# Kernel tuning notes

Measured on AMD Instinct MI355X. Metric: run time of the kernel, lower is better.

Reference implementation:

```python
import jax, jax.numpy as jnp
import numpy as np

N = 50000      # nodes
E = 800000     # edges (no self-loops; loops added in forward)
D = 128        # input_dim == nb_hidden_gnn
K = 128        # nb_hidden_kernel
EMB = 128      # emb_dim
L = 3          # nb_layer
EPS = 1e-5


def setup_inputs() -> dict:
    key = jax.random.key(0)
    ks = jax.random.split(key, 14)
    x = jax.random.normal(ks[0], (N, D), dtype=jnp.float32)
    src = jax.random.randint(ks[1], (E,), 0, N)
    dst = jax.random.randint(ks[2], (E,), 0, N)
    dst = jnp.where(src == dst, (dst + 1) % N, dst)  # guarantee no self-loops
    edge_index = jnp.stack([src, dst]).astype(jnp.int32)
    edge_attr = jax.random.uniform(ks[3], (E,), dtype=jnp.float32)
    s = 0.05
    # stacked per-layer params (layer 0..L-1): in=out=D for all layers
    lin_w = jax.random.normal(ks[4], (L, D, 2 * D), dtype=jnp.float32) * s
    lin_b = jax.random.normal(ks[5], (L, D), dtype=jnp.float32) * s
    linA_w = jax.random.normal(ks[6], (L, K, 2 * D + 1), dtype=jnp.float32) * s
    linA_b = jax.random.normal(ks[7], (L, K), dtype=jnp.float32) * s
    linB_w = jax.random.normal(ks[8], (L, K), dtype=jnp.float32) * s
    linB_b = jax.random.normal(ks[9], (L,), dtype=jnp.float32) * s
    # batchnorm affine params for layers 1..L-1
    bn_gamma = jnp.ones((L - 1, D), dtype=jnp.float32)
    bn_beta = jnp.zeros((L - 1, D), dtype=jnp.float32)
    final_w = jax.random.normal(ks[10], (EMB, D), dtype=jnp.float32) * s
    final_b = jax.random.normal(ks[11], (EMB,), dtype=jnp.float32) * s
    return {"x": x, "edge_index": edge_index, "edge_attr": edge_attr,
            "lin_w": lin_w, "lin_b": lin_b,
            "linA_w": linA_w, "linA_b": linA_b,
            "linB_w": linB_w, "linB_b": linB_b,
            "bn_gamma": bn_gamma, "bn_beta": bn_beta,
            "final_w": final_w, "final_b": final_b}


def _batchnorm(h, gamma, beta):
    mean = jnp.mean(h, axis=0)
    var = jnp.mean(jnp.square(h - mean), axis=0)  # biased, training mode
    return (h - mean) * jax.lax.rsqrt(var + EPS) * gamma + beta


def _gcn_layer(h, src, dst, attr, lw, lb, law, lab, lbw, lbb):
    # gather endpoint features: x_i = target, x_j = source
    x_i = h[dst]                                   # [Eall, D]
    x_j = h[src]                                   # [Eall, D]
    e = jnp.concatenate([x_i, x_j, attr[:, None]], axis=1)  # [Eall, 2D+1]
    hk = jax.nn.relu(e @ law.T + lab)              # [Eall, K]
    w = jax.nn.sigmoid(hk @ lbw + lbb)             # [Eall]
    msg = w[:, None] * x_j                         # gated message
    prop = jax.ops.segment_sum(msg, dst, num_segments=N)  # scatter-add to targets
    return jax.nn.relu(jnp.concatenate([h, prop], axis=1) @ lw.T + lb)


def reference(x, edge_index, edge_attr, lin_w, lin_b, linA_w, linA_b,
              linB_w, linB_b, bn_gamma, bn_beta, final_w, final_b):
    loop = jnp.arange(N, dtype=edge_index.dtype)
    src = jnp.concatenate([edge_index[0], loop])   # add self-loops
    dst = jnp.concatenate([edge_index[1], loop])
    attr = jnp.concatenate([edge_attr, jnp.zeros((N,), edge_attr.dtype)])  # fill_value=0
    h = x
    for i in range(L):
        if i > 0:
            h = _batchnorm(h, bn_gamma[i - 1], bn_beta[i - 1])
        h = _gcn_layer(h, src, dst, attr, lin_w[i], lin_b[i],
                       linA_w[i], linA_b[i], linB_w[i], linB_b[i])
    return h @ final_w.T + final_b
```

## Files before the change

### kernel.cpp

```cpp
#include <hip/hip_runtime.h>

#define EPSBN 1e-5f
#define CAP 64

typedef __attribute__((ext_vector_type(8))) short bf16x8;
typedef __attribute__((ext_vector_type(4))) float f32x4;
typedef __attribute__((ext_vector_type(2))) float f32x2;
typedef __attribute__((ext_vector_type(4))) unsigned int u32x4;

__device__ inline unsigned short f2bf(float f) {
    unsigned u = __builtin_bit_cast(unsigned, f);
    return (unsigned short)((u + 0x7FFFu + ((u >> 16) & 1u)) >> 16);
}
__device__ inline unsigned pack2(float a, float b) {
    return (unsigned)f2bf(a) | ((unsigned)f2bf(b) << 16);
}
__device__ inline float bf2f_lo(unsigned v) { return __builtin_bit_cast(float, v << 16); }
__device__ inline float bf2f_hi(unsigned v) { return __builtin_bit_cast(float, v & 0xFFFF0000u); }
__device__ inline f32x2 bf2f2(unsigned v) {
    f32x2 r; r.x = bf2f_lo(v); r.y = bf2f_hi(v); return r;
}

__global__ void k_wall(const float* __restrict__ linA_w, const float* __restrict__ lin_w,
                       const float* __restrict__ fw, unsigned short* __restrict__ WB,
                       float* __restrict__ AC, int* __restrict__ cursor,
                       float* __restrict__ sums, int N) {
    int y = blockIdx.y;
    int i = blockIdx.x * 256 + threadIdx.x;
    if (y == 14) {
        if (i < N) cursor[i] = 0;
        else if (i < N + 512) sums[i - N] = 0.f;
        return;
    }
    if (y == 13) {
        if (i < 384) {
            int l = i >> 7, k = i & 127;
            AC[i] = linA_w[(size_t)l * 32896 + (size_t)k * 257 + 256];
        }
        return;
    }
    if (i >= 16384) return;
    int r = i >> 7, c = i & 127;
    const float* sp;
    int stride, coloff;
    if (y < 3)       { sp = linA_w + (size_t)y * 32896;       stride = 257; coloff = 0; }
    else if (y < 6)  { sp = linA_w + (size_t)(y - 3) * 32896; stride = 257; coloff = 128; }
    else if (y < 9)  { sp = lin_w + (size_t)(y - 6) * 32768;  stride = 256; coloff = 0; }
    else if (y < 12) { sp = lin_w + (size_t)(y - 9) * 32768;  stride = 256; coloff = 128; }
    else             { sp = fw;                               stride = 128; coloff = 0; }
    WB[(size_t)y * 16384 + i] = f2bf(sp[(size_t)r * stride + coloff + c]);
}

__global__ void k_scatter(const int* __restrict__ src, const int* __restrict__ dst,
                          const float* __restrict__ attr, int* __restrict__ cursor,
                          int2* __restrict__ cedge, int E, int E4) {
    int e = blockIdx.x * blockDim.x + threadIdx.x;
    if (e >= E4) return;
#pragma unroll
    for (int r = 0; r < 4; ++r) {
        int idx = e + r * E4;
        if (idx < E) {
            int d = dst[idx];
            int pos = atomicAdd(&cursor[d], 1);
            if (pos < CAP) cedge[((size_t)d << 6) + pos] = make_int2(src[idx], __float_as_int(attr[idx]));
        }
    }
}

__global__ __launch_bounds__(256) void k_pq(const float* __restrict__ xf32,
                                            const float* __restrict__ sums,
                                            const float* __restrict__ gamma,
                                            const float* __restrict__ beta, float invN,
                                            unsigned short* __restrict__ QH,
                                            const unsigned short* __restrict__ BtP,
                                            const unsigned short* __restrict__ BtQ,
                                            const float* __restrict__ lab,
                                            unsigned short* __restrict__ PB, int M) {
    __shared__ unsigned short As[16384];
    __shared__ float sbn[256];
    int t = threadIdx.x;
    int m0 = blockIdx.x << 7;
    if (sums) {
        if (t < 128) {
            float mean = sums[t] * invN;
            float var = sums[128 + t] * invN - mean * mean;
            float sc = gamma[t] * rsqrtf(var + EPSBN);
            sbn[t] = sc;
            sbn[128 + t] = beta[t] - mean * sc;
        }
        __syncthreads();
    }
    {
        int r = t >> 1, hk = t & 1;
        int gm = m0 + r;
        if (gm < M) {
            unsigned short* hrow = QH + (size_t)gm * 256 + 128 + hk * 64;
            if (xf32) {
                const float* xr = xf32 + (size_t)gm * 128 + hk * 64;
#pragma unroll
                for (int c = 0; c < 8; ++c) {
                    float4 lo = *(const float4*)(xr + c * 8);
                    float4 hi = *(const float4*)(xr + c * 8 + 4);
                    u32x4 u;
                    u[0] = pack2(lo.x, lo.y); u[1] = pack2(lo.z, lo.w);
                    u[2] = pack2(hi.x, hi.y); u[3] = pack2(hi.z, hi.w);
                    *(u32x4*)&As[(((hk * 8 + c) * 128) + r) * 8] = u;
                    *(u32x4*)(hrow + c * 8) = u;
                }
            } else {
#pragma unroll
                for (int c = 0; c < 8; ++c) {
                    u32x4 u = *(const u32x4*)(hrow + c * 8);
                    int k = hk * 64 + c * 8;
                    float4 sc0 = *(const float4*)(sbn + k);
                    float4 sc1 = *(const float4*)(sbn + k + 4);
                    float4 sh0 = *(const float4*)(sbn + 128 + k);
                    float4 sh1 = *(const float4*)(sbn + 128 + k + 4);
                    u32x4 o;
                    o[0] = pack2(bf2f_lo(u[0]) * sc0.x + sh0.x, bf2f_hi(u[0]) * sc0.y + sh0.y);
                    o[1] = pack2(bf2f_lo(u[1]) * sc0.z + sh0.z, bf2f_hi(u[1]) * sc0.w + sh0.w);
                    o[2] = pack2(bf2f_lo(u[2]) * sc1.x + sh1.x, bf2f_hi(u[2]) * sc1.y + sh1.y);
                    o[3] = pack2(bf2f_lo(u[3]) * sc1.z + sh1.z, bf2f_hi(u[3]) * sc1.w + sh1.w);
                    *(u32x4*)&As[(((hk * 8 + c) * 128) + r) * 8] = o;
                    *(u32x4*)(hrow + c * 8) = o;
                }
            }
        }
    }
    __syncthreads();
    int lane = t & 63;
    int wvi = t >> 6, wr = wvi >> 1, wc = wvi & 1;
    int sub = lane & 15, kg = lane >> 4;
#pragma unroll
    for (int pass = 0; pass < 2; ++pass) {
        const unsigned short* Bt = pass ? BtQ : BtP;
        bf16x8 bfr[4][4];
#pragma unroll
        for (int s = 0; s < 4; ++s)
#pragma unroll
            for (int n = 0; n < 4; ++n) {
                int col = wc * 64 + n * 16 + sub;
                bfr[s][n] = *(const bf16x8*)(Bt + (size_t)col * 128 + s * 32 + kg * 8);
            }
        f32x4 acc[4][4];
#pragma unroll
        for (int m = 0; m < 4; ++m)
#pragma unroll
            for (int n = 0; n < 4; ++n) acc[m][n] = (f32x4){0.f, 0.f, 0.f, 0.f};
#pragma unroll
        for (int s = 0; s < 4; ++s) {
            bf16x8 a[4];
#pragma unroll
            for (int m = 0; m < 4; ++m) {
                int row = wr * 64 + m * 16 + sub;
                a[m] = *(const bf16x8*)&As[(((s * 4 + kg) * 128) + row) * 8];
            }
#pragma unroll
            for (int m = 0; m < 4; ++m)
#pragma unroll
                for (int n = 0; n < 4; ++n)
                    acc[m][n] = __builtin_amdgcn_mfma_f32_16x16x32_bf16(bfr[s][n], a[m],
                                                                        acc[m][n], 0, 0, 0);
        }
#pragma unroll
        for (int m = 0; m < 4; ++m) {
            int lr = wr * 64 + m * 16 + sub;
            int gr = m0 + lr;
            if (gr < M) {
#pragma unroll
                for (int n = 0; n < 4; ++n) {
                    int gc0 = wc * 64 + n * 16 + kg * 4;
                    ushort4 o;
                    if (pass) {
                        o.x = f2bf(acc[m][n][0]); o.y = f2bf(acc[m][n][1]);
                        o.z = f2bf(acc[m][n][2]); o.w = f2bf(acc[m][n][3]);
                        *(ushort4*)(QH + (size_t)gr * 256 + gc0) = o;
                    } else {
                        float4 bv = *(const float4*)(lab + gc0);
                        o.x = f2bf(acc[m][n][0] + bv.x); o.y = f2bf(acc[m][n][1] + bv.y);
                        o.z = f2bf(acc[m][n][2] + bv.z); o.w = f2bf(acc[m][n][3] + bv.w);
                        *(ushort4*)(PB + (size_t)gr * 128 + gc0) = o;
                    }
                }
            }
        }
    }
}

__global__ __launch_bounds__(256) void k_mm(const unsigned short* __restrict__ A0, int sA0,
                                            const unsigned short* __restrict__ Bt0,
                                            const unsigned short* __restrict__ A1,
                                            const unsigned short* __restrict__ Bt1,
                                            const float* __restrict__ bias,
                                            unsigned short* __restrict__ Chb,
                                            float* __restrict__ sums,
                                            const unsigned short* __restrict__ BtF,
                                            const float* __restrict__ fbias,
                                            float* __restrict__ outF,
                                            int M, int relu) {
    __shared__ unsigned short As[16384];
    __shared__ float sbuf[256];
    int t = threadIdx.x;
    if (sums) sbuf[t] = 0.f;
    int m0 = blockIdx.x << 7;
    int lane = t & 63;
    int wvi = t >> 6, wr = wvi >> 1, wc = wvi & 1;
    int sub = lane & 15, kg = lane >> 4;
    f32x4 acc[4][4];
#pragma unroll
    for (int m = 0; m < 4; ++m)
#pragma unroll
        for (int n = 0; n < 4; ++n) acc[m][n] = (f32x4){0.f, 0.f, 0.f, 0.f};
#pragma unroll
    for (int pass = 0; pass < 2; ++pass) {
        const unsigned short* A = pass ? A1 : A0;
        int sA = pass ? 128 : sA0;
        const unsigned short* Bt = pass ? Bt1 : Bt0;
        if (pass) __syncthreads();
        {
            int r = t >> 1, hk = t & 1;
            int gm = m0 + r;
            if (gm < M) {
                const unsigned short* arow = A + (size_t)gm * sA + hk * 64;
#pragma unroll
                for (int c = 0; c < 8; ++c) {
                    u32x4 u = *(const u32x4*)(arow + c * 8);
                    *(u32x4*)&As[(((hk * 8 + c) * 128) + r) * 8] = u;
                }
            }
        }
        bf16x8 bfr[4][4];
#pragma unroll
        for (int s = 0; s < 4; ++s)
#pragma unroll
            for (int n = 0; n < 4; ++n) {
                int col = wc * 64 + n * 16 + sub;
                bfr[s][n] = *(const bf16x8*)(Bt + (size_t)col * 128 + s * 32 + kg * 8);
            }
        __syncthreads();
#pragma unroll
        for (int s = 0; s < 4; ++s) {
            bf16x8 a[4];
#pragma unroll
            for (int m = 0; m < 4; ++m) {
                int row = wr * 64 + m * 16 + sub;
                a[m] = *(const bf16x8*)&As[(((s * 4 + kg) * 128) + row) * 8];
            }
#pragma unroll
            for (int m = 0; m < 4; ++m)
#pragma unroll
                for (int n = 0; n < 4; ++n)
                    acc[m][n] = __builtin_amdgcn_mfma_f32_16x16x32_bf16(bfr[s][n], a[m],
                                                                        acc[m][n], 0, 0, 0);
        }
    }
    f32x4 s1[4], s2[4];
#pragma unroll
    for (int n = 0; n < 4; ++n) { s1[n] = (f32x4){0.f, 0.f, 0.f, 0.f}; s2[n] = s1[n]; }
#pragma unroll
    for (int m = 0; m < 4; ++m) {
        int gr = m0 + wr * 64 + m * 16 + sub;
        bool ok = gr < M;
#pragma unroll
        for (int n = 0; n < 4; ++n) {
            int gc0 = wc * 64 + n * 16 + kg * 4;
            float4 bv = *(const float4*)(bias + gc0);
            acc[m][n][0] += bv.x; acc[m][n][1] += bv.y;
            acc[m][n][2] += bv.z; acc[m][n][3] += bv.w;
            if (relu) {
#pragma unroll
                for (int e = 0; e < 4; ++e) acc[m][n][e] = fmaxf(acc[m][n][e], 0.f);
            }
            if (sums && ok) { s1[n] += acc[m][n]; s2[n] += acc[m][n] * acc[m][n]; }
        }
    }
    if (sums) {
#pragma unroll
        for (int n = 0; n < 4; ++n)
#pragma unroll
            for (int e = 0; e < 4; ++e) {
#pragma unroll
                for (int mask = 1; mask < 16; mask <<= 1) {
                    s1[n][e] += __shfl_xor(s1[n][e], mask, 64);
                    s2[n][e] += __shfl_xor(s2[n][e], mask, 64);
                }
            }
        if (sub == 0) {
#pragma unroll
            for (int n = 0; n < 4; ++n) {
                int gc0 = wc * 64 + n * 16 + kg * 4;
#pragma unroll
                for (int e = 0; e < 4; ++e) {
                    atomicAdd(&sbuf[gc0 + e], s1[n][e]);
                    atomicAdd(&sbuf[128 + gc0 + e], s2[n][e]);
                }
            }
        }
    }
    if (!BtF) {
#pragma unroll
        for (int m = 0; m < 4; ++m) {
            int gr = m0 + wr * 64 + m * 16 + sub;
            if (gr < M) {
#pragma unroll
                for (int n = 0; n < 4; ++n) {
                    int gc0 = wc * 64 + n * 16 + kg * 4;
                    ushort4 o;
                    o.x = f2bf(acc[m][n][0]); o.y = f2bf(acc[m][n][1]);
                    o.z = f2bf(acc[m][n][2]); o.w = f2bf(acc[m][n][3]);
                    *(ushort4*)(Chb + (size_t)gr * 256 + gc0) = o;
                }
            }
        }
    } else {
        __syncthreads();
#pragma unroll
        for (int m = 0; m < 4; ++m) {
            int lr = wr * 64 + m * 16 + sub;
#pragma unroll
            for (int n = 0; n < 4; ++n) {
                int gc0 = wc * 64 + n * 16 + kg * 4;
                ushort4 o;
                o.x = f2bf(acc[m][n][0]); o.y = f2bf(acc[m][n][1]);
                o.z = f2bf(acc[m][n][2]); o.w = f2bf(acc[m][n][3]);
                *(ushort4*)&As[(((gc0 >> 3) * 128) + lr) * 8 + (gc0 & 7)] = o;
            }
        }
        bf16x8 bfrF[4][4];
#pragma unroll
        for (int s = 0; s < 4; ++s)
#pragma unroll
            for (int n = 0; n < 4; ++n) {
                int col = wc * 64 + n * 16 + sub;
                bfrF[s][n] = *(const bf16x8*)(BtF + (size_t)col * 128 + s * 32 + kg * 8);
            }
        __syncthreads();
        f32x4 acc2[4][4];
#pragma unroll
        for (int m = 0; m < 4; ++m)
#pragma unroll
            for (int n = 0; n < 4; ++n) acc2[m][n] = (f32x4){0.f, 0.f, 0.f, 0.f};
#pragma unroll
        for (int s = 0; s < 4; ++s) {
            bf16x8 a[4];
#pragma unroll
            for (int m = 0; m < 4; ++m) {
                int row = wr * 64 + m * 16 + sub;
                a[m] = *(const bf16x8*)&As[(((s * 4 + kg) * 128) + row) * 8];
            }
#pragma unroll
            for (int m = 0; m < 4; ++m)
#pragma unroll
                for (int n = 0; n < 4; ++n)
                    acc2[m][n] = __builtin_amdgcn_mfma_f32_16x16x32_bf16(bfrF[s][n], a[m],
                                                                         acc2[m][n], 0, 0, 0);
        }
#pragma unroll
        for (int m = 0; m < 4; ++m) {
            int gr = m0 + wr * 64 + m * 16 + sub;
            if (gr < M) {
#pragma unroll
                for (int n = 0; n < 4; ++n) {
                    int gc0 = wc * 64 + n * 16 + kg * 4;
                    float4 fb = *(const float4*)(fbias + gc0);
                    float4 o;
                    o.x = acc2[m][n][0] + fb.x; o.y = acc2[m][n][1] + fb.y;
                    o.z = acc2[m][n][2] + fb.z; o.w = acc2[m][n][3] + fb.w;
                    *(float4*)(outF + (size_t)gr * 128 + gc0) = o;
                }
            }
        }
    }
    if (sums) {
        __syncthreads();
        atomicAdd(&sums[t], sbuf[t]);
    }
}

__global__ __launch_bounds__(128) void k_edge(const unsigned short* __restrict__ QH,
                                              const unsigned short* __restrict__ PB,
                                              const float* __restrict__ acv,
                                              const float* __restrict__ lbw,
                                              const float* __restrict__ lbbp,
                                              const int* __restrict__ deg,
                                              const int2* __restrict__ cedge,
                                              unsigned short* __restrict__ prop, int N) {
    int wid = (blockIdx.x * 128 + threadIdx.x) >> 6;
    if (wid >= N) return;
    int lane = threadIdx.x & 63;
    int sub = lane & 15;
    int g = lane >> 4;
    int ks = sub * 8;
    f32x2 p2[4], wv2[4], ac2[4];
    {
        u32x4 pv = *(const u32x4*)(PB + (size_t)wid * 128 + ks);
#pragma unroll
        for (int i = 0; i < 4; ++i) p2[i] = bf2f2(pv[i]);
        float4 w0 = *(const float4*)(lbw + ks), w1 = *(const float4*)(lbw + ks + 4);
        wv2[0] = (f32x2){w0.x, w0.y}; wv2[1] = (f32x2){w0.z, w0.w};
        wv2[2] = (f32x2){w1.x, w1.y}; wv2[3] = (f32x2){w1.z, w1.w};
        float4 c0 = *(const float4*)(acv + ks), c1 = *(const float4*)(acv + ks + 4);
        ac2[0] = (f32x2){c0.x, c0.y}; ac2[1] = (f32x2){c0.z, c0.w};
        ac2[2] = (f32x2){c1.x, c1.y}; ac2[3] = (f32x2){c1.z, c1.w};
    }
    float lbb = lbbp[0];
    const int2* row = cedge + ((size_t)wid << 6);
    int cnt = min(deg[wid], CAP) + 1;
    int s0 = wid, s1 = wid, s2 = wid;
    float a0 = 0.f, a1 = 0.f, a2 = 0.f;
    {
        int id = g;
        if (id > 0 && id < cnt) { int2 ed = row[id - 1]; s0 = ed.x; a0 = __int_as_float(ed.y); }
    }
    {
        int id = 4 + g;
        if (id < cnt) { int2 ed = row[id - 1]; s1 = ed.x; a1 = __int_as_float(ed.y); }
    }
    {
        int id = 8 + g;
        if (id < cnt) { int2 ed = row[id - 1]; s2 = ed.x; a2 = __int_as_float(ed.y); }
    }
    u32x4 q0 = *(const u32x4*)(QH + (size_t)s0 * 256 + ks);
    u32x4 q1 = *(const u32x4*)(QH + (size_t)s1 * 256 + ks);
    u32x4 h0 = *(const u32x4*)(QH + (size_t)s0 * 256 + 128 + ks);
    f32x2 acc2[4];
#pragma unroll
    for (int i = 0; i < 4; ++i) acc2[i] = (f32x2){0.f, 0.f};
    const f32x2 z2 = (f32x2){0.f, 0.f};
    for (int base = 0; base < cnt; base += 4) {
        int s3 = wid; float a3 = 0.f;
        {
            int id = base + 12 + g;
            if (id < cnt) { int2 ed = row[id - 1]; s3 = ed.x; a3 = __int_as_float(ed.y); }
        }
        u32x4 q2 = *(const u32x4*)(QH + (size_t)s2 * 256 + ks);
        u32x4 h1 = *(const u32x4*)(QH + (size_t)s1 * 256 + 128 + ks);
        f32x2 ts2 = z2;
#pragma unroll
        for (int i = 0; i < 4; ++i) {
            f32x2 tv = ac2[i] * a0 + p2[i] + bf2f2(q0[i]);
            tv = __builtin_elementwise_max(tv, z2);
            ts2 += wv2[i] * tv;
        }
        float ts = ts2.x + ts2.y;
        ts += __shfl_xor(ts, 1, 16);
        ts += __shfl_xor(ts, 2, 16);
        ts += __shfl_xor(ts, 4, 16);
        ts += __shfl_xor(ts, 8, 16);
        float w = 1.f / (1.f + __expf(-(ts + lbb)));
        if (base + g < cnt) {
#pragma unroll
            for (int i = 0; i < 4; ++i) acc2[i] += w * bf2f2(h0[i]);
        }
        s0 = s1; a0 = a1; s1 = s2; a1 = a2; s2 = s3; a2 = a3;
        q0 = q1; q1 = q2; h0 = h1;
    }
#pragma unroll
    for (int j = 0; j < 4; ++j) {
        acc2[j].x += __shfl_xor(acc2[j].x, 16, 64);
        acc2[j].y += __shfl_xor(acc2[j].y, 16, 64);
        acc2[j].x += __shfl_xor(acc2[j].x, 32, 64);
        acc2[j].y += __shfl_xor(acc2[j].y, 32, 64);
    }
    if (g == 0) {
        u32x4 o;
        o[0] = pack2(acc2[0].x, acc2[0].y);
        o[1] = pack2(acc2[1].x, acc2[1].y);
        o[2] = pack2(acc2[2].x, acc2[2].y);
        o[3] = pack2(acc2[3].x, acc2[3].y);
        *(u32x4*)(prop + (size_t)wid * 128 + ks) = o;
    }
}

extern "C" void kernel_launch(void* const* d_in, const int* in_sizes, int n_in,
                              void* d_out, int out_size, void* d_ws, size_t ws_size,
                              hipStream_t stream) {
    const float* x      = (const float*)d_in[0];
    const int*   ei     = (const int*)d_in[1];
    const float* eattr  = (const float*)d_in[2];
    const float* lin_w  = (const float*)d_in[3];
    const float* lin_b  = (const float*)d_in[4];
    const float* linA_w = (const float*)d_in[5];
    const float* linA_b = (const float*)d_in[6];
    const float* linB_w = (const float*)d_in[7];
    const float* linB_b = (const float*)d_in[8];
    const float* bn_g   = (const float*)d_in[9];
    const float* bn_b   = (const float*)d_in[10];
    const float* fw     = (const float*)d_in[11];
    const float* fb     = (const float*)d_in[12];

    int N = in_sizes[0] / 128;
    int E = in_sizes[1] / 2;
    const int* src = ei;
    const int* dst = ei + E;
    int E4 = (E + 3) / 4;

    size_t off = 0;
    auto alloc = [&](size_t bytes) {
        void* p = (char*)d_ws + off;
        off += (bytes + 255) & ~255ULL;
        return p;
    };
    unsigned short* QH = (unsigned short*)alloc((size_t)N * 256 * 2);
    unsigned short* PB = (unsigned short*)alloc((size_t)N * 128 * 2);
    unsigned short* PR = (unsigned short*)alloc((size_t)N * 128 * 2);
    int* cursor  = (int*)alloc((size_t)N * 4);
    float* sums  = (float*)alloc(2 * 256 * 4);
    int2* cedge  = (int2*)alloc((size_t)N * CAP * 8);
    unsigned short* WB = (unsigned short*)alloc((size_t)13 * 16384 * 2);
    float* AC = (float*)alloc(384 * 4);

    {
        int nx = (N + 512 + 255) / 256;
        if (nx < 64) nx = 64;
        dim3 gw(nx, 15);
        k_wall<<<gw, 256, 0, stream>>>(linA_w, lin_w, fw, WB, AC, cursor, sums, N);
    }
    k_scatter<<<(E4 + 255) / 256, 256, 0, stream>>>(src, dst, eattr, cursor, cedge, E, E4);

    unsigned short* BP = WB;
    unsigned short* BQ = WB + 3 * 16384;
    unsigned short* BU0 = WB + 6 * 16384;
    unsigned short* BU1 = WB + 9 * 16384;
    unsigned short* BF = WB + 12 * 16384;

    int gemmGrid = (N + 127) / 128;

    for (int l = 0; l < 3; ++l) {
        k_pq<<<gemmGrid, 256, 0, stream>>>(l ? nullptr : x,
                                           l ? sums + (size_t)(l - 1) * 256 : nullptr,
                                           l ? bn_g + (size_t)(l - 1) * 128 : nullptr,
                                           l ? bn_b + (size_t)(l - 1) * 128 : nullptr,
                                           1.f / N, QH,
                                           BP + (size_t)l * 16384, BQ + (size_t)l * 16384,
                                           linA_b + (size_t)l * 128, PB, N);
        k_edge<<<(N * 64 + 127) / 128, 128, 0, stream>>>(QH, PB,
                                                         AC + (size_t)l * 128,
                                                         linB_w + (size_t)l * 128,
                                                         linB_b + l,
                                                         cursor, cedge, PR, N);
        if (l < 2) {
            k_mm<<<gemmGrid, 256, 0, stream>>>(QH + 128, 256, BU0 + (size_t)l * 16384,
                                               PR, BU1 + (size_t)l * 16384,
                                               lin_b + (size_t)l * 128,
                                               QH + 128, sums + (size_t)l * 256,
                                               nullptr, nullptr, nullptr, N, 1);
        } else {
            k_mm<<<gemmGrid, 256, 0, stream>>>(QH + 128, 256, BU0 + (size_t)l * 16384,
                                               PR, BU1 + (size_t)l * 16384,
                                               lin_b + (size_t)l * 128,
                                               nullptr, nullptr, BF, fb, (float*)d_out, N, 1);
        }
    }
}
```

Before: 406.3 us.

## Fuse edge bucketing into first PQ GEMM launch and halve GEMM row tiles

Removes the separate scatter kernel and appends its blocks to the layer-0 k_pq grid, so edge bucketing runs alongside the first node GEMM. The k_pq and k_mm tiles shrink from 128 to 64 rows per block, doubling block count and halving LDS use. Weight fragments are now loaded inside the k-loop instead of being preloaded into registers. The intent is better occupancy and overlap on a small N, at the cost of more redundant weight loads per row.

```diff
diff --git a/kernel.cpp b/kernel.cpp
--- a/kernel.cpp
+++ b/kernel.cpp
@@ -51,22 +51,6 @@
     WB[(size_t)y * 16384 + i] = f2bf(sp[(size_t)r * stride + coloff + c]);
 }
 
-__global__ void k_scatter(const int* __restrict__ src, const int* __restrict__ dst,
-                          const float* __restrict__ attr, int* __restrict__ cursor,
-                          int2* __restrict__ cedge, int E, int E4) {
-    int e = blockIdx.x * blockDim.x + threadIdx.x;
-    if (e >= E4) return;
-#pragma unroll
-    for (int r = 0; r < 4; ++r) {
-        int idx = e + r * E4;
-        if (idx < E) {
-            int d = dst[idx];
-            int pos = atomicAdd(&cursor[d], 1);
-            if (pos < CAP) cedge[((size_t)d << 6) + pos] = make_int2(src[idx], __float_as_int(attr[idx]));
-        }
-    }
-}
-
 __global__ __launch_bounds__(256) void k_pq(const float* __restrict__ xf32,
                                             const float* __restrict__ sums,
                                             const float* __restrict__ gamma,
@@ -75,11 +59,33 @@
                                             const unsigned short* __restrict__ BtP,
                                             const unsigned short* __restrict__ BtQ,
                                             const float* __restrict__ lab,
-                                            unsigned short* __restrict__ PB, int M) {
-    __shared__ unsigned short As[16384];
+                                            unsigned short* __restrict__ PB, int M, int npq,
+                                            const int* __restrict__ esrc,
+                                            const int* __restrict__ edst,
+                                            const float* __restrict__ eattr,
+                                            int* __restrict__ cursor,
+                                            int2* __restrict__ cedge, int E, int E4) {
+    __shared__ unsigned short As[64 * 128];
     __shared__ float sbn[256];
+    int bid = blockIdx.x;
     int t = threadIdx.x;
-    int m0 = blockIdx.x << 7;
+    if (bid >= npq) {
+        int e = (bid - npq) * 256 + t;
+        if (e < E4) {
+#pragma unroll
+            for (int r = 0; r < 4; ++r) {
+                int idx = e + r * E4;
+                if (idx < E) {
+                    int d = edst[idx];
+                    int pos = atomicAdd(&cursor[d], 1);
+                    if (pos < CAP)
+                        cedge[((size_t)d << 6) + pos] = make_int2(esrc[idx], __float_as_int(eattr[idx]));
+                }
+            }
+        }
+        return;
+    }
+    int m0 = bid << 6;
     if (sums) {
         if (t < 128) {
             float mean = sums[t] * invN;
@@ -91,27 +97,28 @@
         __syncthreads();
     }
     {
-        int r = t >> 1, hk = t & 1;
+        int r = t >> 2, qk = t & 3;
         int gm = m0 + r;
         if (gm < M) {
-            unsigned short* hrow = QH + (size_t)gm * 256 + 128 + hk * 64;
+            unsigned short* hrow = QH + (size_t)gm * 256 + 128;
             if (xf32) {
-                const float* xr = xf32 + (size_t)gm * 128 + hk * 64;
-#pragma unroll
-                for (int c = 0; c < 8; ++c) {
-                    float4 lo = *(const float4*)(xr + c * 8);
-                    float4 hi = *(const float4*)(xr + c * 8 + 4);
+                const float* xr = xf32 + (size_t)gm * 128;
+#pragma unroll
+                for (int c = 0; c < 4; ++c) {
+                    int k = qk * 32 + c * 8;
+                    float4 lo = *(const float4*)(xr + k);
+                    float4 hi = *(const float4*)(xr + k + 4);
                     u32x4 u;
                     u[0] = pack2(lo.x, lo.y); u[1] = pack2(lo.z, lo.w);
                     u[2] = pack2(hi.x, hi.y); u[3] = pack2(hi.z, hi.w);
-                    *(u32x4*)&As[(((hk * 8 + c) * 128) + r) * 8] = u;
-                    *(u32x4*)(hrow + c * 8) = u;
+                    *(u32x4*)&As[(((qk * 4 + c) * 64) + r) * 8] = u;
+                    *(u32x4*)(hrow + k) = u;
                 }
             } else {
 #pragma unroll
-                for (int c = 0; c < 8; ++c) {
-                    u32x4 u = *(const u32x4*)(hrow + c * 8);
-                    int k = hk * 64 + c * 8;
+                for (int c = 0; c < 4; ++c) {
+                    int k = qk * 32 + c * 8;
+                    u32x4 u = *(const u32x4*)(hrow + k);
                     float4 sc0 = *(const float4*)(sbn + k);
                     float4 sc1 = *(const float4*)(sbn + k + 4);
                     float4 sh0 = *(const float4*)(sbn + 128 + k);
@@ -121,8 +128,8 @@
                     o[1] = pack2(bf2f_lo(u[1]) * sc0.z + sh0.z, bf2f_hi(u[1]) * sc0.w + sh0.w);
                     o[2] = pack2(bf2f_lo(u[2]) * sc1.x + sh1.x, bf2f_hi(u[2]) * sc1.y + sh1.y);
                     o[3] = pack2(bf2f_lo(u[3]) * sc1.z + sh1.z, bf2f_hi(u[3]) * sc1.w + sh1.w);
-                    *(u32x4*)&As[(((hk * 8 + c) * 128) + r) * 8] = o;
-                    *(u32x4*)(hrow + c * 8) = o;
+                    *(u32x4*)&As[(((qk * 4 + c) * 64) + r) * 8] = o;
+                    *(u32x4*)(hrow + k) = o;
                 }
             }
         }
@@ -134,38 +141,32 @@
 #pragma unroll
     for (int pass = 0; pass < 2; ++pass) {
         const unsigned short* Bt = pass ? BtQ : BtP;
-        bf16x8 bfr[4][4];
-#pragma unroll
-        for (int s = 0; s < 4; ++s)
+        f32x4 acc[2][4];
+#pragma unroll
+        for (int m = 0; m < 2; ++m)
+#pragma unroll
+            for (int n = 0; n < 4; ++n) acc[m][n] = (f32x4){0.f, 0.f, 0.f, 0.f};
+#pragma unroll
+        for (int s = 0; s < 4; ++s) {
+            bf16x8 a[2];
+#pragma unroll
+            for (int m = 0; m < 2; ++m) {
+                int row = wr * 32 + m * 16 + sub;
+                a[m] = *(const bf16x8*)&As[(((s * 4 + kg) * 64) + row) * 8];
+            }
 #pragma unroll
             for (int n = 0; n < 4; ++n) {
                 int col = wc * 64 + n * 16 + sub;
-                bfr[s][n] = *(const bf16x8*)(Bt + (size_t)col * 128 + s * 32 + kg * 8);
-            }
-        f32x4 acc[4][4];
-#pragma unroll
-        for (int m = 0; m < 4; ++m)
-#pragma unroll
-            for (int n = 0; n < 4; ++n) acc[m][n] = (f32x4){0.f, 0.f, 0.f, 0.f};
-#pragma unroll
-        for (int s = 0; s < 4; ++s) {
-            bf16x8 a[4];
-#pragma unroll
-            for (int m = 0; m < 4; ++m) {
-                int row = wr * 64 + m * 16 + sub;
-                a[m] = *(const bf16x8*)&As[(((s * 4 + kg) * 128) + row) * 8];
-            }
-#pragma unroll
-            for (int m = 0; m < 4; ++m)
-#pragma unroll
-                for (int n = 0; n < 4; ++n)
-                    acc[m][n] = __builtin_amdgcn_mfma_f32_16x16x32_bf16(bfr[s][n], a[m],
+                bf16x8 b = *(const bf16x8*)(Bt + (size_t)col * 128 + s * 32 + kg * 8);
+#pragma unroll
+                for (int m = 0; m < 2; ++m)
+                    acc[m][n] = __builtin_amdgcn_mfma_f32_16x16x32_bf16(b, a[m],
                                                                         acc[m][n], 0, 0, 0);
-        }
-#pragma unroll
-        for (int m = 0; m < 4; ++m) {
-            int lr = wr * 64 + m * 16 + sub;
-            int gr = m0 + lr;
+            }
+        }
+#pragma unroll
+        for (int m = 0; m < 2; ++m) {
+            int gr = m0 + wr * 32 + m * 16 + sub;
             if (gr < M) {
 #pragma unroll
                 for (int n = 0; n < 4; ++n) {
@@ -198,17 +199,17 @@
                                             const float* __restrict__ fbias,
                                             float* __restrict__ outF,
                                             int M, int relu) {
-    __shared__ unsigned short As[16384];
+    __shared__ unsigned short As[64 * 128];
     __shared__ float sbuf[256];
     int t = threadIdx.x;
     if (sums) sbuf[t] = 0.f;
-    int m0 = blockIdx.x << 7;
+    int m0 = blockIdx.x << 6;
     int lane = t & 63;
     int wvi = t >> 6, wr = wvi >> 1, wc = wvi & 1;
     int sub = lane & 15, kg = lane >> 4;
-    f32x4 acc[4][4];
-#pragma unroll
-    for (int m = 0; m < 4; ++m)
+    f32x4 acc[2][4];
+#pragma unroll
+    for (int m = 0; m < 2; ++m)
 #pragma unroll
         for (int n = 0; n < 4; ++n) acc[m][n] = (f32x4){0.f, 0.f, 0.f, 0.f};
 #pragma unroll
@@ -218,48 +219,43 @@
         const unsigned short* Bt = pass ? Bt1 : Bt0;
         if (pass) __syncthreads();
         {
-            int r = t >> 1, hk = t & 1;
+            int r = t >> 2, qk = t & 3;
             int gm = m0 + r;
             if (gm < M) {
-                const unsigned short* arow = A + (size_t)gm * sA + hk * 64;
-#pragma unroll
-                for (int c = 0; c < 8; ++c) {
+                const unsigned short* arow = A + (size_t)gm * sA + qk * 32;
+#pragma unroll
+                for (int c = 0; c < 4; ++c) {
                     u32x4 u = *(const u32x4*)(arow + c * 8);
-                    *(u32x4*)&As[(((hk * 8 + c) * 128) + r) * 8] = u;
-                }
-            }
-        }
-        bf16x8 bfr[4][4];
-#pragma unroll
-        for (int s = 0; s < 4; ++s)
+                    *(u32x4*)&As[(((qk * 4 + c) * 64) + r) * 8] = u;
+                }
+            }
+        }
+        __syncthreads();
+#pragma unroll
+        for (int s = 0; s < 4; ++s) {
+            bf16x8 a[2];
+#pragma unroll
+            for (int m = 0; m < 2; ++m) {
+                int row = wr * 32 + m * 16 + sub;
+                a[m] = *(const bf16x8*)&As[(((s * 4 + kg) * 64) + row) * 8];
+            }
 #pragma unroll
             for (int n = 0; n < 4; ++n) {
                 int col = wc * 64 + n * 16 + sub;
-                bfr[s][n] = *(const bf16x8*)(Bt + (size_t)col * 128 + s * 32 + kg * 8);
-            }
-        __syncthreads();
-#pragma unroll
-        for (int s = 0; s < 4; ++s) {
-            bf16x8 a[4];
-#pragma unroll
-            for (int m = 0; m < 4; ++m) {
-                int row = wr * 64 + m * 16 + sub;
-                a[m] = *(const bf16x8*)&As[(((s * 4 + kg) * 128) + row) * 8];
-            }
-#pragma unroll
-            for (int m = 0; m < 4; ++m)
-#pragma unroll
-                for (int n = 0; n < 4; ++n)
-                    acc[m][n] = __builtin_amdgcn_mfma_f32_16x16x32_bf16(bfr[s][n], a[m],
+                bf16x8 b = *(const bf16x8*)(Bt + (size_t)col * 128 + s * 32 + kg * 8);
+#pragma unroll
+                for (int m = 0; m < 2; ++m)
+                    acc[m][n] = __builtin_amdgcn_mfma_f32_16x16x32_bf16(b, a[m],
                                                                         acc[m][n], 0, 0, 0);
+            }
         }
     }
     f32x4 s1[4], s2[4];
 #pragma unroll
     for (int n = 0; n < 4; ++n) { s1[n] = (f32x4){0.f, 0.f, 0.f, 0.f}; s2[n] = s1[n]; }
 #pragma unroll
-    for (int m = 0; m < 4; ++m) {
-        int gr = m0 + wr * 64 + m * 16 + sub;
+    for (int m = 0; m < 2; ++m) {
+        int gr = m0 + wr * 32 + m * 16 + sub;
         bool ok = gr < M;
 #pragma unroll
         for (int n = 0; n < 4; ++n) {
@@ -299,8 +295,8 @@
     }
     if (!BtF) {
 #pragma unroll
-        for (int m = 0; m < 4; ++m) {
-            int gr = m0 + wr * 64 + m * 16 + sub;
+        for (int m = 0; m < 2; ++m) {
+            int gr = m0 + wr * 32 + m * 16 + sub;
             if (gr < M) {
 #pragma unroll
                 for (int n = 0; n < 4; ++n) {
@@ -315,49 +311,44 @@
     } else {
         __syncthreads();
 #pragma unroll
-        for (int m = 0; m < 4; ++m) {
-            int lr = wr * 64 + m * 16 + sub;
+        for (int m = 0; m < 2; ++m) {
+            int lr = wr * 32 + m * 16 + sub;
 #pragma unroll
             for (int n = 0; n < 4; ++n) {
                 int gc0 = wc * 64 + n * 16 + kg * 4;
                 ushort4 o;
                 o.x = f2bf(acc[m][n][0]); o.y = f2bf(acc[m][n][1]);
                 o.z = f2bf(acc[m][n][2]); o.w = f2bf(acc[m][n][3]);
-                *(ushort4*)&As[(((gc0 >> 3) * 128) + lr) * 8 + (gc0 & 7)] = o;
-            }
-        }
-        bf16x8 bfrF[4][4];
-#pragma unroll
-        for (int s = 0; s < 4; ++s)
+                *(ushort4*)&As[(((gc0 >> 3) * 64) + lr) * 8 + (gc0 & 7)] = o;
+            }
+        }
+        __syncthreads();
+        f32x4 acc2[2][4];
+#pragma unroll
+        for (int m = 0; m < 2; ++m)
+#pragma unroll
+            for (int n = 0; n < 4; ++n) acc2[m][n] = (f32x4){0.f, 0.f, 0.f, 0.f};
+#pragma unroll
+        for (int s = 0; s < 4; ++s) {
+            bf16x8 a[2];
+#pragma unroll
+            for (int m = 0; m < 2; ++m) {
+                int row = wr * 32 + m * 16 + sub;
+                a[m] = *(const bf16x8*)&As[(((s * 4 + kg) * 64) + row) * 8];
+            }
 #pragma unroll
             for (int n = 0; n < 4; ++n) {
                 int col = wc * 64 + n * 16 + sub;
-                bfrF[s][n] = *(const bf16x8*)(BtF + (size_t)col * 128 + s * 32 + kg * 8);
-            }
-        __syncthreads();
-        f32x4 acc2[4][4];
-#pragma unroll
-        for (int m = 0; m < 4; ++m)
-#pragma unroll
-            for (int n = 0; n < 4; ++n) acc2[m][n] = (f32x4){0.f, 0.f, 0.f, 0.f};
-#pragma unroll
-        for (int s = 0; s < 4; ++s) {
-            bf16x8 a[4];
-#pragma unroll
-            for (int m = 0; m < 4; ++m) {
-                int row = wr * 64 + m * 16 + sub;
-                a[m] = *(const bf16x8*)&As[(((s * 4 + kg) * 128) + row) * 8];
-            }
-#pragma unroll
-            for (int m = 0; m < 4; ++m)
-#pragma unroll
-                for (int n = 0; n < 4; ++n)
-                    acc2[m][n] = __builtin_amdgcn_mfma_f32_16x16x32_bf16(bfrF[s][n], a[m],
+                bf16x8 b = *(const bf16x8*)(BtF + (size_t)col * 128 + s * 32 + kg * 8);
+#pragma unroll
+                for (int m = 0; m < 2; ++m)
+                    acc2[m][n] = __builtin_amdgcn_mfma_f32_16x16x32_bf16(b, a[m],
                                                                          acc2[m][n], 0, 0, 0);
-        }
-#pragma unroll
-        for (int m = 0; m < 4; ++m) {
-            int gr = m0 + wr * 64 + m * 16 + sub;
+            }
+        }
+#pragma unroll
+        for (int m = 0; m < 2; ++m) {
+            int gr = m0 + wr * 32 + m * 16 + sub;
             if (gr < M) {
 #pragma unroll
                 for (int n = 0; n < 4; ++n) {
@@ -516,7 +507,6 @@
         dim3 gw(nx, 15);
         k_wall<<<gw, 256, 0, stream>>>(linA_w, lin_w, fw, WB, AC, cursor, sums, N);
     }
-    k_scatter<<<(E4 + 255) / 256, 256, 0, stream>>>(src, dst, eattr, cursor, cedge, E, E4);
 
     unsigned short* BP = WB;
     unsigned short* BQ = WB + 3 * 16384;
@@ -524,16 +514,19 @@
     unsigned short* BU1 = WB + 9 * 16384;
     unsigned short* BF = WB + 12 * 16384;
 
-    int gemmGrid = (N + 127) / 128;
+    int gemmGrid = (N + 63) / 64;
+    int sblocks = (E4 + 255) / 256;
 
     for (int l = 0; l < 3; ++l) {
-        k_pq<<<gemmGrid, 256, 0, stream>>>(l ? nullptr : x,
-                                           l ? sums + (size_t)(l - 1) * 256 : nullptr,
-                                           l ? bn_g + (size_t)(l - 1) * 128 : nullptr,
-                                           l ? bn_b + (size_t)(l - 1) * 128 : nullptr,
-                                           1.f / N, QH,
-                                           BP + (size_t)l * 16384, BQ + (size_t)l * 16384,
-                                           linA_b + (size_t)l * 128, PB, N);
+        int grid = gemmGrid + (l == 0 ? sblocks : 0);
+        k_pq<<<grid, 256, 0, stream>>>(l ? nullptr : x,
+                                       l ? sums + (size_t)(l - 1) * 256 : nullptr,
+                                       l ? bn_g + (size_t)(l - 1) * 128 : nullptr,
+                                       l ? bn_b + (size_t)(l - 1) * 128 : nullptr,
+                                       1.f / N, QH,
+                                       BP + (size_t)l * 16384, BQ + (size_t)l * 16384,
+                                       linA_b + (size_t)l * 128, PB, N, gemmGrid,
+                                       src, dst, eattr, cursor, cedge, E, E4);
         k_edge<<<(N * 64 + 127) / 128, 128, 0, stream>>>(QH, PB,
                                                          AC + (size_t)l * 128,
                                                          linB_w + (size_t)l * 128,
```

Result: slower. 453.2 us (+11.5%).
